# Kernel optimization log

Hardware: AMD Instinct MI355X
Metric: run time of the kernel (lower is better)

Reference implementation:

```python
import jax, jax.numpy as jnp
import numpy as np


def setup_inputs() -> dict:
    key = jax.random.key(0)
    ks = jax.random.split(key, 5)
    N, C, W, H = 16, 256, 32, 32
    scale = 1.0 / np.sqrt(C)
    return {
        "x": jax.random.normal(ks[0], (N, C, W, H), dtype=jnp.float32),
        "w_theta": jax.random.normal(ks[1], (C, C), dtype=jnp.float32) * scale,
        "w_phi": jax.random.normal(ks[2], (C, C), dtype=jnp.float32) * scale,
        "w_g": jax.random.normal(ks[3], (C, C), dtype=jnp.float32) * scale,
        "w_restore": jax.random.normal(ks[4], (C, C), dtype=jnp.float32) * scale,
    }


def reference(x, w_theta, w_phi, w_g, w_restore):
    N, C, W, H = x.shape
    L = W * H
    xf = x.reshape(N, C, L)  # [N, C, L]
    # 1x1 convs == channel-mixing matmuls
    t = jnp.einsum('ac,ncl->nal', w_theta, xf)  # theta(x), [N, A, L]
    p = jnp.einsum('ac,ncl->nal', w_phi, xf)    # phi(x),   [N, A, L]
    g = jnp.einsum('ac,ncl->nal', w_g, xf)      # g(x),     [N, A, L]
    # c = x1 @ x2 with x1 = theta(x)^T : [N, L, L]
    c = jnp.einsum('nai,naj->nij', t, p)
    # GLOBAL softmax over the entire flattened L*L map per sample (not per-row)
    a = jax.nn.softmax(c.reshape(N, L * L), axis=1).reshape(N, L, L)
    # attn = g(x) @ a : [N, A, L] -> [N, A, W, H]
    attn = jnp.einsum('nai,nij->naj', g, a).reshape(N, C, W, H)
    # restore 1x1 conv back to in_features
    attn = jnp.einsum('ca,nawh->ncwh', w_restore, attn)
    return (c, x + attn)
```

## Files before the change

kernel.cpp:

```cpp
#include <hip/hip_runtime.h>
#include <hip/hip_bf16.h>

#define N_ 16
#define C_ 256
#define L_ 1024
#define LL_ (L_ * L_)
#define M0 128.0f

using bf16 = __hip_bfloat16;
typedef __bf16 bf16x8 __attribute__((ext_vector_type(8)));
typedef float f32x4 __attribute__((ext_vector_type(4)));

__device__ __forceinline__ float b2f(bf16 v) { return __bfloat162float(v); }
__device__ __forceinline__ bf16 f2b(float v) { return __float2bfloat16(v); }

__device__ __forceinline__ unsigned packb2(float a, float b) {
    union { bf16 h; unsigned short u; } ua, ub;
    ua.h = f2b(a); ub.h = f2b(b);
    return (unsigned)ua.u | ((unsigned)ub.u << 16);
}

__device__ __forceinline__ float waveRedSum(float v) {
#pragma unroll
    for (int o = 32; o > 0; o >>= 1) v += __shfl_down(v, o, 64);
    return v;
}

__global__ void k_init(const float* __restrict__ wt, const float* __restrict__ wp,
                       const float* __restrict__ wg, const float* __restrict__ wr,
                       bf16* __restrict__ Wstack, float* __restrict__ sumv) {
    int b = blockIdx.x, t = threadIdx.x;
    if (b < 512) {
        int i = b * 256 + t;
        const float* src = (b < 256 ? wt : wp);
        Wstack[i] = f2b(src[i & 65535]);
    } else {
        int row = b - 512;
        const float* wrr = wr + row * 256;
        float acc = 0.f;
#pragma unroll 8
        for (int k = 0; k < 256; ++k) acc += wrr[k] * wg[k * 256 + t];
        Wstack[(size_t)b * 256 + t] = f2b(acc);
    }
    if (b == 0 && t < N_) sumv[t] = 0.f;
}

__global__ void __launch_bounds__(256) k_trans(const float* __restrict__ src,
                                               bf16* __restrict__ dst) {
    __shared__ unsigned sh[128 * 65];
    int n = blockIdx.z;
    int r0 = blockIdx.y * 128, c0 = blockIdx.x * 128;
    int t = threadIdx.x;
    const float* sp = src + (size_t)n * C_ * L_;
#pragma unroll
    for (int pass = 0; pass < 16; ++pass) {
        int idx = pass * 256 + t;
        int row = idx >> 5, cf4 = idx & 31;
        float4 v = *reinterpret_cast<const float4*>(
            sp + (size_t)(r0 + row) * L_ + c0 + cf4 * 4);
        sh[row * 65 + cf4 * 2]     = packb2(v.x, v.y);
        sh[row * 65 + cf4 * 2 + 1] = packb2(v.z, v.w);
    }
    __syncthreads();
    bf16* dp = dst + (size_t)n * L_ * C_;
#pragma unroll
    for (int pass = 0; pass < 8; ++pass) {
        int idx = pass * 256 + t;
        int ig = (idx & 3) + 4 * (idx >> 9);
        int jl = (idx >> 2) & 127;
        unsigned ow[4];
#pragma unroll
        for (int dpair = 0; dpair < 4; ++dpair) {
            int il = ig * 8 + dpair * 2;
            unsigned w0 = sh[il * 65 + (jl >> 1)];
            unsigned w1 = sh[(il + 1) * 65 + (jl >> 1)];
            unsigned a = (jl & 1) ? (w0 >> 16) : (w0 & 0xffffu);
            unsigned b = (jl & 1) ? (w1 >> 16) : (w1 & 0xffffu);
            ow[dpair] = a | (b << 16);
        }
        uint4 o; o.x = ow[0]; o.y = ow[1]; o.z = ow[2]; o.w = ow[3];
        *reinterpret_cast<uint4*>(dp + (size_t)(c0 + jl) * C_ + r0 + ig * 8) = o;
    }
}

__global__ void __launch_bounds__(256) k_tpg(const bf16* __restrict__ Wstack,
                                             const bf16* __restrict__ xT,
                                             bf16* __restrict__ tT, bf16* __restrict__ pT,
                                             bf16* __restrict__ gW) {
    __shared__ bf16 As[128 * 32];
    __shared__ bf16 Bs[128 * 32];
    const int t = threadIdx.x;
    const int lane = t & 63, wid = t >> 6;
    const int wr = wid >> 1, wc = wid & 1;
    const int q = lane >> 4, ln = lane & 15;
    const int l0 = blockIdx.x * 128, mt = blockIdx.y, n = blockIdx.z;
    const bf16* Ab = Wstack + (size_t)mt * 128 * C_;
    const bf16* Bb = xT + ((size_t)n * L_ + l0) * C_;
    const int sr = t >> 2, sk = (t & 3) * 8;

    f32x4 acc[4][4] = {};
    for (int kb = 0; kb < C_; kb += 32) {
        uint4 a0v = *reinterpret_cast<const uint4*>(Ab + (size_t)sr * C_ + kb + sk);
        uint4 a1v = *reinterpret_cast<const uint4*>(Ab + (size_t)(sr + 64) * C_ + kb + sk);
        uint4 b0v = *reinterpret_cast<const uint4*>(Bb + (size_t)sr * C_ + kb + sk);
        uint4 b1v = *reinterpret_cast<const uint4*>(Bb + (size_t)(sr + 64) * C_ + kb + sk);
        *reinterpret_cast<uint4*>(&As[t * 8])         = a0v;
        *reinterpret_cast<uint4*>(&As[(t + 256) * 8]) = a1v;
        *reinterpret_cast<uint4*>(&Bs[t * 8])         = b0v;
        *reinterpret_cast<uint4*>(&Bs[(t + 256) * 8]) = b1v;
        __syncthreads();
        bf16x8 af[4], bfr[4];
#pragma unroll
        for (int mi = 0; mi < 4; ++mi)
            af[mi] = *reinterpret_cast<const bf16x8*>(&As[(wr * 64 + mi * 16 + ln) * 32 + q * 8]);
#pragma unroll
        for (int ni = 0; ni < 4; ++ni)
            bfr[ni] = *reinterpret_cast<const bf16x8*>(&Bs[(wc * 64 + ni * 16 + ln) * 32 + q * 8]);
#pragma unroll
        for (int mi = 0; mi < 4; ++mi)
#pragma unroll
            for (int ni = 0; ni < 4; ++ni)
                acc[mi][ni] = __builtin_amdgcn_mfma_f32_16x16x32_bf16(af[mi], bfr[ni], acc[mi][ni], 0, 0, 0);
        __syncthreads();
    }
    int kind = mt >> 1;
    int mbase = (mt & 1) * 128;
    if (kind == 2) {
        bf16* ob = gW + (size_t)n * C_ * L_;
#pragma unroll
        for (int mi = 0; mi < 4; ++mi) {
            int a = mbase + wr * 64 + mi * 16 + q * 4;
#pragma unroll
            for (int ni = 0; ni < 4; ++ni) {
                int l = l0 + wc * 64 + ni * 16 + ln;
#pragma unroll
                for (int r = 0; r < 4; ++r)
                    ob[(size_t)(a + r) * L_ + l] = f2b(acc[mi][ni][r]);
            }
        }
    } else {
        bf16* ob = (kind == 0 ? tT : pT) + (size_t)n * L_ * C_;
#pragma unroll
        for (int mi = 0; mi < 4; ++mi) {
            int a = mbase + wr * 64 + mi * 16 + q * 4;
#pragma unroll
            for (int ni = 0; ni < 4; ++ni) {
                int l = l0 + wc * 64 + ni * 16 + ln;
                bf16 tmp[4];
#pragma unroll
                for (int r = 0; r < 4; ++r) tmp[r] = f2b(acc[mi][ni][r]);
                *reinterpret_cast<uint2*>(ob + (size_t)l * C_ + a) =
                    *reinterpret_cast<const uint2*>(tmp);
            }
        }
    }
}

__global__ void __launch_bounds__(256) k_cmat(const bf16* __restrict__ tT,
                                              const bf16* __restrict__ pT,
                                              float* __restrict__ cout,
                                              bf16* __restrict__ eT,
                                              float* __restrict__ sumv) {
    __shared__ bf16 As[128 * 32];
    __shared__ bf16 Bs[128 * 32];
    const int t = threadIdx.x;
    const int lane = t & 63, wid = t >> 6;
    const int wr = wid >> 1, wc = wid & 1;
    const int q = lane >> 4, ln = lane & 15;
    const int j0 = blockIdx.x * 128, i0 = blockIdx.y * 128, n = blockIdx.z;
    const bf16* Ab = tT + ((size_t)n * L_ + i0) * C_;
    const bf16* Bb = pT + ((size_t)n * L_ + j0) * C_;
    const int sr = t >> 2, sk = (t & 3) * 8;

    f32x4 acc[4][4] = {};
    for (int kb = 0; kb < C_; kb += 32) {
        uint4 a0v = *reinterpret_cast<const uint4*>(Ab + (size_t)sr * C_ + kb + sk);
        uint4 a1v = *reinterpret_cast<const uint4*>(Ab + (size_t)(sr + 64) * C_ + kb + sk);
        uint4 b0v = *reinterpret_cast<const uint4*>(Bb + (size_t)sr * C_ + kb + sk);
        uint4 b1v = *reinterpret_cast<const uint4*>(Bb + (size_t)(sr + 64) * C_ + kb + sk);
        *reinterpret_cast<uint4*>(&As[t * 8])         = a0v;
        *reinterpret_cast<uint4*>(&As[(t + 256) * 8]) = a1v;
        *reinterpret_cast<uint4*>(&Bs[t * 8])         = b0v;
        *reinterpret_cast<uint4*>(&Bs[(t + 256) * 8]) = b1v;
        __syncthreads();
        bf16x8 af[4], bfr[4];
#pragma unroll
        for (int mi = 0; mi < 4; ++mi)
            af[mi] = *reinterpret_cast<const bf16x8*>(&As[(wr * 64 + mi * 16 + ln) * 32 + q * 8]);
#pragma unroll
        for (int ni = 0; ni < 4; ++ni)
            bfr[ni] = *reinterpret_cast<const bf16x8*>(&Bs[(wc * 64 + ni * 16 + ln) * 32 + q * 8]);
#pragma unroll
        for (int mi = 0; mi < 4; ++mi)
#pragma unroll
            for (int ni = 0; ni < 4; ++ni)
                acc[mi][ni] = __builtin_amdgcn_mfma_f32_16x16x32_bf16(af[mi], bfr[ni], acc[mi][ni], 0, 0, 0);
        __syncthreads();
    }
    float s = 0.f;
    float* cb = cout + (size_t)n * LL_;
    bf16*  ep = eT + (size_t)n * LL_;
#pragma unroll
    for (int mi = 0; mi < 4; ++mi) {
        int i = i0 + wr * 64 + mi * 16 + q * 4;
#pragma unroll
        for (int ni = 0; ni < 4; ++ni) {
            int j = j0 + wc * 64 + ni * 16 + ln;
            bf16 tmp[4];
#pragma unroll
            for (int r = 0; r < 4; ++r) {
                float v = acc[mi][ni][r];
                cb[(size_t)(i + r) * L_ + j] = v;
                float e = __expf(v - M0);
                s += e;
                tmp[r] = f2b(e);
            }
            *reinterpret_cast<uint2*>(ep + (size_t)j * L_ + i) =
                *reinterpret_cast<const uint2*>(tmp);
        }
    }
    __shared__ float sh[4];
    s = waveRedSum(s);
    if (lane == 0) sh[wid] = s;
    __syncthreads();
    if (t == 0) atomicAdd(&sumv[n], sh[0] + sh[1] + sh[2] + sh[3]);
}

__global__ void __launch_bounds__(256) k_out(const bf16* __restrict__ gW,
                                             const bf16* __restrict__ eT,
                                             const float* __restrict__ sumv,
                                             const float* __restrict__ x,
                                             float* __restrict__ out) {
    __shared__ bf16 As[128 * 32];
    __shared__ bf16 Bs[128 * 32];
    const int t = threadIdx.x;
    const int lane = t & 63, wid = t >> 6;
    const int wr = wid >> 1, wc = wid & 1;
    const int q = lane >> 4, ln = lane & 15;
    const int j0 = blockIdx.x * 128, c0 = blockIdx.y * 128, n = blockIdx.z;
    const bf16* Ab = gW + ((size_t)n * C_ + c0) * L_;
    const bf16* Bb = eT + ((size_t)n * L_ + j0) * L_;
    const int sr = t >> 2, sk = (t & 3) * 8;

    f32x4 acc[4][4] = {};
    for (int kb = 0; kb < L_; kb += 32) {
        uint4 a0v = *reinterpret_cast<const uint4*>(Ab + (size_t)sr * L_ + kb + sk);
        uint4 a1v = *reinterpret_cast<const uint4*>(Ab + (size_t)(sr + 64) * L_ + kb + sk);
        uint4 b0v = *reinterpret_cast<const uint4*>(Bb + (size_t)sr * L_ + kb + sk);
        uint4 b1v = *reinterpret_cast<const uint4*>(Bb + (size_t)(sr + 64) * L_ + kb + sk);
        *reinterpret_cast<uint4*>(&As[t * 8])         = a0v;
        *reinterpret_cast<uint4*>(&As[(t + 256) * 8]) = a1v;
        *reinterpret_cast<uint4*>(&Bs[t * 8])         = b0v;
        *reinterpret_cast<uint4*>(&Bs[(t + 256) * 8]) = b1v;
        __syncthreads();
        bf16x8 af[4], bfr[4];
#pragma unroll
        for (int mi = 0; mi < 4; ++mi)
            af[mi] = *reinterpret_cast<const bf16x8*>(&As[(wr * 64 + mi * 16 + ln) * 32 + q * 8]);
#pragma unroll
        for (int ni = 0; ni < 4; ++ni)
            bfr[ni] = *reinterpret_cast<const bf16x8*>(&Bs[(wc * 64 + ni * 16 + ln) * 32 + q * 8]);
#pragma unroll
        for (int mi = 0; mi < 4; ++mi)
#pragma unroll
            for (int ni = 0; ni < 4; ++ni)
                acc[mi][ni] = __builtin_amdgcn_mfma_f32_16x16x32_bf16(af[mi], bfr[ni], acc[mi][ni], 0, 0, 0);
        __syncthreads();
    }
    float inv = 1.0f / sumv[n];
    const float* xb = x + (size_t)n * C_ * L_;
    float* ob = out + (size_t)n * C_ * L_;
#pragma unroll
    for (int mi = 0; mi < 4; ++mi) {
        int c = c0 + wr * 64 + mi * 16 + q * 4;
#pragma unroll
        for (int ni = 0; ni < 4; ++ni) {
            int j = j0 + wc * 64 + ni * 16 + ln;
#pragma unroll
            for (int r = 0; r < 4; ++r) {
                size_t off = (size_t)(c + r) * L_ + j;
                ob[off] = acc[mi][ni][r] * inv + xb[off];
            }
        }
    }
}

extern "C" void kernel_launch(void* const* d_in, const int* in_sizes, int n_in,
                              void* d_out, int out_size, void* d_ws, size_t ws_size,
                              hipStream_t stream) {
    const float* x  = (const float*)d_in[0];
    const float* wt = (const float*)d_in[1];
    const float* wp = (const float*)d_in[2];
    const float* wg = (const float*)d_in[3];
    const float* wr = (const float*)d_in[4];

    float* out_c = (float*)d_out;
    float* out_y = out_c + (size_t)N_ * LL_;

    bf16* tTb = (bf16*)out_y;
    bf16* pTb = tTb + (size_t)N_ * L_ * C_;

    char* base = (char*)d_ws;
    float* sumv   = (float*)base;
    bf16*  Wstack = (bf16*)(base + 1024);
    bf16*  xTb    = Wstack + 768 * 256;
    bf16*  gWb    = xTb + (size_t)N_ * L_ * C_;
    bf16*  eTb    = gWb + (size_t)N_ * C_ * L_;

    k_init<<<dim3(768), dim3(256), 0, stream>>>(wt, wp, wg, wr, Wstack, sumv);
    k_trans<<<dim3(8, 2, 16), dim3(256), 0, stream>>>(x, xTb);
    k_tpg<<<dim3(8, 6, 16), dim3(256), 0, stream>>>(Wstack, xTb, tTb, pTb, gWb);
    k_cmat<<<dim3(8, 8, 16), dim3(256), 0, stream>>>(tTb, pTb, out_c, eTb, sumv);
    k_out<<<dim3(8, 2, 16), dim3(256), 0, stream>>>(gWb, eTb, sumv, x, out_y);
}
```

Baseline: 183.0 us.

## Use direct global-to-LDS loads, double-buffer k_out, merge init and transpose kernels

```diff
diff --git a/kernel.cpp b/kernel.cpp
--- a/kernel.cpp
+++ b/kernel.cpp
@@ -14,6 +14,12 @@
 __device__ __forceinline__ float b2f(bf16 v) { return __bfloat162float(v); }
 __device__ __forceinline__ bf16 f2b(float v) { return __float2bfloat16(v); }
 
+__device__ __forceinline__ void glds16(const bf16* g, bf16* l) {
+    __builtin_amdgcn_global_load_lds(
+        (const __attribute__((address_space(1))) void*)g,
+        (__attribute__((address_space(3))) void*)l, 16, 0, 0);
+}
+
 __device__ __forceinline__ unsigned packb2(float a, float b) {
     union { bf16 h; unsigned short u; } ua, ub;
     ua.h = f2b(a); ub.h = f2b(b);
@@ -26,32 +32,37 @@
     return v;
 }
 
-__global__ void k_init(const float* __restrict__ wt, const float* __restrict__ wp,
-                       const float* __restrict__ wg, const float* __restrict__ wr,
-                       bf16* __restrict__ Wstack, float* __restrict__ sumv) {
+__global__ void __launch_bounds__(256) k_prep(const float* __restrict__ wt,
+                                              const float* __restrict__ wp,
+                                              const float* __restrict__ wg,
+                                              const float* __restrict__ wr,
+                                              const float* __restrict__ x,
+                                              bf16* __restrict__ Wstack,
+                                              bf16* __restrict__ xT,
+                                              float* __restrict__ sumv) {
+    __shared__ unsigned sh[128 * 65];
     int b = blockIdx.x, t = threadIdx.x;
-    if (b < 512) {
-        int i = b * 256 + t;
-        const float* src = (b < 256 ? wt : wp);
-        Wstack[i] = f2b(src[i & 65535]);
-    } else {
-        int row = b - 512;
-        const float* wrr = wr + row * 256;
-        float acc = 0.f;
+    if (b < 768) {
+        if (b < 512) {
+            int i = b * 256 + t;
+            const float* src = (b < 256 ? wt : wp);
+            Wstack[i] = f2b(src[i & 65535]);
+        } else {
+            int row = b - 512;
+            const float* wrr = wr + row * 256;
+            float acc = 0.f;
 #pragma unroll 8
-        for (int k = 0; k < 256; ++k) acc += wrr[k] * wg[k * 256 + t];
-        Wstack[(size_t)b * 256 + t] = f2b(acc);
-    }
-    if (b == 0 && t < N_) sumv[t] = 0.f;
-}
-
-__global__ void __launch_bounds__(256) k_trans(const float* __restrict__ src,
-                                               bf16* __restrict__ dst) {
-    __shared__ unsigned sh[128 * 65];
-    int n = blockIdx.z;
-    int r0 = blockIdx.y * 128, c0 = blockIdx.x * 128;
-    int t = threadIdx.x;
-    const float* sp = src + (size_t)n * C_ * L_;
+            for (int k = 0; k < 256; ++k) acc += wrr[k] * wg[k * 256 + t];
+            Wstack[(size_t)b * 256 + t] = f2b(acc);
+        }
+        if (b == 0 && t < N_) sumv[t] = 0.f;
+        return;
+    }
+    int bb = b - 768;
+    int c0 = (bb & 7) * 128;
+    int r0 = ((bb >> 3) & 1) * 128;
+    int n = bb >> 4;
+    const float* sp = x + (size_t)n * C_ * L_;
 #pragma unroll
     for (int pass = 0; pass < 16; ++pass) {
         int idx = pass * 256 + t;
@@ -62,7 +73,7 @@
         sh[row * 65 + cf4 * 2 + 1] = packb2(v.z, v.w);
     }
     __syncthreads();
-    bf16* dp = dst + (size_t)n * L_ * C_;
+    bf16* dp = xT + (size_t)n * L_ * C_;
 #pragma unroll
     for (int pass = 0; pass < 8; ++pass) {
         int idx = pass * 256 + t;
@@ -75,8 +86,8 @@
             unsigned w0 = sh[il * 65 + (jl >> 1)];
             unsigned w1 = sh[(il + 1) * 65 + (jl >> 1)];
             unsigned a = (jl & 1) ? (w0 >> 16) : (w0 & 0xffffu);
-            unsigned b = (jl & 1) ? (w1 >> 16) : (w1 & 0xffffu);
-            ow[dpair] = a | (b << 16);
+            unsigned bv = (jl & 1) ? (w1 >> 16) : (w1 & 0xffffu);
+            ow[dpair] = a | (bv << 16);
         }
         uint4 o; o.x = ow[0]; o.y = ow[1]; o.z = ow[2]; o.w = ow[3];
         *reinterpret_cast<uint4*>(dp + (size_t)(c0 + jl) * C_ + r0 + ig * 8) = o;
@@ -87,8 +98,8 @@
                                              const bf16* __restrict__ xT,
                                              bf16* __restrict__ tT, bf16* __restrict__ pT,
                                              bf16* __restrict__ gW) {
-    __shared__ bf16 As[128 * 32];
-    __shared__ bf16 Bs[128 * 32];
+    __shared__ __align__(16) bf16 As[128 * 32];
+    __shared__ __align__(16) bf16 Bs[128 * 32];
     const int t = threadIdx.x;
     const int lane = t & 63, wid = t >> 6;
     const int wr = wid >> 1, wc = wid & 1;
@@ -97,17 +108,17 @@
     const bf16* Ab = Wstack + (size_t)mt * 128 * C_;
     const bf16* Bb = xT + ((size_t)n * L_ + l0) * C_;
     const int sr = t >> 2, sk = (t & 3) * 8;
+    bf16* AsW0 = &As[(size_t)(wid * 64) * 8];
+    bf16* AsW1 = &As[(size_t)(wid * 64 + 256) * 8];
+    bf16* BsW0 = &Bs[(size_t)(wid * 64) * 8];
+    bf16* BsW1 = &Bs[(size_t)(wid * 64 + 256) * 8];
 
     f32x4 acc[4][4] = {};
     for (int kb = 0; kb < C_; kb += 32) {
-        uint4 a0v = *reinterpret_cast<const uint4*>(Ab + (size_t)sr * C_ + kb + sk);
-        uint4 a1v = *reinterpret_cast<const uint4*>(Ab + (size_t)(sr + 64) * C_ + kb + sk);
-        uint4 b0v = *reinterpret_cast<const uint4*>(Bb + (size_t)sr * C_ + kb + sk);
-        uint4 b1v = *reinterpret_cast<const uint4*>(Bb + (size_t)(sr + 64) * C_ + kb + sk);
-        *reinterpret_cast<uint4*>(&As[t * 8])         = a0v;
-        *reinterpret_cast<uint4*>(&As[(t + 256) * 8]) = a1v;
-        *reinterpret_cast<uint4*>(&Bs[t * 8])         = b0v;
-        *reinterpret_cast<uint4*>(&Bs[(t + 256) * 8]) = b1v;
+        glds16(Ab + (size_t)sr * C_ + kb + sk, AsW0);
+        glds16(Ab + (size_t)(sr + 64) * C_ + kb + sk, AsW1);
+        glds16(Bb + (size_t)sr * C_ + kb + sk, BsW0);
+        glds16(Bb + (size_t)(sr + 64) * C_ + kb + sk, BsW1);
         __syncthreads();
         bf16x8 af[4], bfr[4];
 #pragma unroll
@@ -161,8 +172,8 @@
                                               float* __restrict__ cout,
                                               bf16* __restrict__ eT,
                                               float* __restrict__ sumv) {
-    __shared__ bf16 As[128 * 32];
-    __shared__ bf16 Bs[128 * 32];
+    __shared__ __align__(16) bf16 As[128 * 32];
+    __shared__ __align__(16) bf16 Bs[128 * 32];
     const int t = threadIdx.x;
     const int lane = t & 63, wid = t >> 6;
     const int wr = wid >> 1, wc = wid & 1;
@@ -171,17 +182,17 @@
     const bf16* Ab = tT + ((size_t)n * L_ + i0) * C_;
     const bf16* Bb = pT + ((size_t)n * L_ + j0) * C_;
     const int sr = t >> 2, sk = (t & 3) * 8;
+    bf16* AsW0 = &As[(size_t)(wid * 64) * 8];
+    bf16* AsW1 = &As[(size_t)(wid * 64 + 256) * 8];
+    bf16* BsW0 = &Bs[(size_t)(wid * 64) * 8];
+    bf16* BsW1 = &Bs[(size_t)(wid * 64 + 256) * 8];
 
     f32x4 acc[4][4] = {};
     for (int kb = 0; kb < C_; kb += 32) {
-        uint4 a0v = *reinterpret_cast<const uint4*>(Ab + (size_t)sr * C_ + kb + sk);
-        uint4 a1v = *reinterpret_cast<const uint4*>(Ab + (size_t)(sr + 64) * C_ + kb + sk);
-        uint4 b0v = *reinterpret_cast<const uint4*>(Bb + (size_t)sr * C_ + kb + sk);
-        uint4 b1v = *reinterpret_cast<const uint4*>(Bb + (size_t)(sr + 64) * C_ + kb + sk);
-        *reinterpret_cast<uint4*>(&As[t * 8])         = a0v;
-        *reinterpret_cast<uint4*>(&As[(t + 256) * 8]) = a1v;
-        *reinterpret_cast<uint4*>(&Bs[t * 8])         = b0v;
-        *reinterpret_cast<uint4*>(&Bs[(t + 256) * 8]) = b1v;
+        glds16(Ab + (size_t)sr * C_ + kb + sk, AsW0);
+        glds16(Ab + (size_t)(sr + 64) * C_ + kb + sk, AsW1);
+        glds16(Bb + (size_t)sr * C_ + kb + sk, BsW0);
+        glds16(Bb + (size_t)(sr + 64) * C_ + kb + sk, BsW1);
         __syncthreads();
         bf16x8 af[4], bfr[4];
 #pragma unroll
@@ -231,8 +242,8 @@
                                              const float* __restrict__ sumv,
                                              const float* __restrict__ x,
                                              float* __restrict__ out) {
-    __shared__ bf16 As[128 * 32];
-    __shared__ bf16 Bs[128 * 32];
+    __shared__ __align__(16) bf16 As[2][128 * 32];
+    __shared__ __align__(16) bf16 Bs[2][128 * 32];
     const int t = threadIdx.x;
     const int lane = t & 63, wid = t >> 6;
     const int wr = wid >> 1, wc = wid & 1;
@@ -241,31 +252,35 @@
     const bf16* Ab = gW + ((size_t)n * C_ + c0) * L_;
     const bf16* Bb = eT + ((size_t)n * L_ + j0) * L_;
     const int sr = t >> 2, sk = (t & 3) * 8;
+    const int w0 = (wid * 64) * 8, w1 = (wid * 64 + 256) * 8;
+
+    auto stage = [&](int kb, int buf) {
+        glds16(Ab + (size_t)sr * L_ + kb + sk, &As[buf][w0]);
+        glds16(Ab + (size_t)(sr + 64) * L_ + kb + sk, &As[buf][w1]);
+        glds16(Bb + (size_t)sr * L_ + kb + sk, &Bs[buf][w0]);
+        glds16(Bb + (size_t)(sr + 64) * L_ + kb + sk, &Bs[buf][w1]);
+    };
 
     f32x4 acc[4][4] = {};
+    stage(0, 0);
+    __syncthreads();
+    int cur = 0;
     for (int kb = 0; kb < L_; kb += 32) {
-        uint4 a0v = *reinterpret_cast<const uint4*>(Ab + (size_t)sr * L_ + kb + sk);
-        uint4 a1v = *reinterpret_cast<const uint4*>(Ab + (size_t)(sr + 64) * L_ + kb + sk);
-        uint4 b0v = *reinterpret_cast<const uint4*>(Bb + (size_t)sr * L_ + kb + sk);
-        uint4 b1v = *reinterpret_cast<const uint4*>(Bb + (size_t)(sr + 64) * L_ + kb + sk);
-        *reinterpret_cast<uint4*>(&As[t * 8])         = a0v;
-        *reinterpret_cast<uint4*>(&As[(t + 256) * 8]) = a1v;
-        *reinterpret_cast<uint4*>(&Bs[t * 8])         = b0v;
-        *reinterpret_cast<uint4*>(&Bs[(t + 256) * 8]) = b1v;
-        __syncthreads();
+        if (kb + 32 < L_) stage(kb + 32, cur ^ 1);
         bf16x8 af[4], bfr[4];
 #pragma unroll
         for (int mi = 0; mi < 4; ++mi)
-            af[mi] = *reinterpret_cast<const bf16x8*>(&As[(wr * 64 + mi * 16 + ln) * 32 + q * 8]);
+            af[mi] = *reinterpret_cast<const bf16x8*>(&As[cur][(wr * 64 + mi * 16 + ln) * 32 + q * 8]);
 #pragma unroll
         for (int ni = 0; ni < 4; ++ni)
-            bfr[ni] = *reinterpret_cast<const bf16x8*>(&Bs[(wc * 64 + ni * 16 + ln) * 32 + q * 8]);
+            bfr[ni] = *reinterpret_cast<const bf16x8*>(&Bs[cur][(wc * 64 + ni * 16 + ln) * 32 + q * 8]);
 #pragma unroll
         for (int mi = 0; mi < 4; ++mi)
 #pragma unroll
             for (int ni = 0; ni < 4; ++ni)
                 acc[mi][ni] = __builtin_amdgcn_mfma_f32_16x16x32_bf16(af[mi], bfr[ni], acc[mi][ni], 0, 0, 0);
         __syncthreads();
+        cur ^= 1;
     }
     float inv = 1.0f / sumv[n];
     const float* xb = x + (size_t)n * C_ * L_;
@@ -307,8 +322,7 @@
     bf16*  gWb    = xTb + (size_t)N_ * L_ * C_;
     bf16*  eTb    = gWb + (size_t)N_ * C_ * L_;
 
-    k_init<<<dim3(768), dim3(256), 0, stream>>>(wt, wp, wg, wr, Wstack, sumv);
-    k_trans<<<dim3(8, 2, 16), dim3(256), 0, stream>>>(x, xTb);
+    k_prep<<<dim3(1024), dim3(256), 0, stream>>>(wt, wp, wg, wr, x, Wstack, xTb, sumv);
     k_tpg<<<dim3(8, 6, 16), dim3(256), 0, stream>>>(Wstack, xTb, tTb, pTb, gWb);
     k_cmat<<<dim3(8, 8, 16), dim3(256), 0, stream>>>(tTb, pTb, out_c, eTb, sumv);
     k_out<<<dim3(8, 2, 16), dim3(256), 0, stream>>>(gWb, eTb, sumv, x, out_y);
```

Measured after the change: 181.1 us. Within noise of the previous version (-1.0%).
